# Optimization experiments

Measured on AMD Instinct MI355X. Metric: run time of the kernel, lower is better.

## Reference

```python
import jax, jax.numpy as jnp
import numpy as np

N_USER = 50000
N_ITEM = 50000
N_EDGE = 800000
D = 128


def _segment_mean(x, idx, num_segments):
    # scatter-mean: sum then divide by in-degree (0 rows stay 0, like PyG mean aggr)
    s = jax.ops.segment_sum(x, idx, num_segments=num_segments)
    cnt = jax.ops.segment_sum(jnp.ones((idx.shape[0], 1), x.dtype), idx, num_segments=num_segments)
    return s / jnp.maximum(cnt, 1.0)


def setup_inputs() -> dict:
    key = jax.random.key(0)
    ks = jax.random.split(key, 11)
    inp = {
        "user_ids": jax.random.randint(ks[0], (N_USER,), 0, N_USER),
        "item_x": jax.random.normal(ks[1], (N_ITEM, D), dtype=jnp.float32),
        "edge_ui": jax.random.randint(ks[2], (2, N_EDGE), 0, N_USER),  # row0: user src, row1: item dst
        "edge_iu": jax.random.randint(ks[3], (2, N_EDGE), 0, N_ITEM),  # row0: item src, row1: user dst
        "user_emb": jax.random.normal(ks[4], (N_USER, D), dtype=jnp.float32),
        "W_l_ui": jax.random.normal(ks[5], (D, D), dtype=jnp.float32) * 0.05,
        "W_r_ui": jax.random.normal(ks[6], (D, D), dtype=jnp.float32) * 0.05,
        "b_ui": jnp.zeros((D,), dtype=jnp.float32),
        "W_l_iu": jax.random.normal(ks[7], (D, D), dtype=jnp.float32) * 0.05,
        "W_r_iu": jax.random.normal(ks[8], (D, D), dtype=jnp.float32) * 0.05,
        "b_iu": jnp.zeros((D,), dtype=jnp.float32),
    }
    return inp


def reference(user_ids, item_x, edge_ui, edge_iu, user_emb,
              W_l_ui, W_r_ui, b_ui, W_l_iu, W_r_iu, b_iu):
    # Embedding lookup for transductive node type 'user'
    x_user = user_emb[user_ids]  # [N_USER, D]

    # SAGEConv for edge type (user -> rates -> item):
    # out_item = lin_l(mean_{j in N(i)} x_user[j]) + lin_r(item_x[i]) + bias
    msg_ui = x_user[edge_ui[0]]                    # gather src features [E, D]
    agg_ui = _segment_mean(msg_ui, edge_ui[1], N_ITEM)
    out_item = agg_ui @ W_l_ui + item_x @ W_r_ui + b_ui

    # SAGEConv for edge type (item -> rev_rates -> user)
    msg_iu = item_x[edge_iu[0]]
    agg_iu = _segment_mean(msg_iu, edge_iu[1], N_USER)
    out_user = agg_iu @ W_l_iu + x_user @ W_r_iu + b_iu

    # HeteroConv aggr='mean' across edge types: each node type is the target of
    # exactly one edge type here, so the cross-edge-type mean is the identity.
    return (out_user, out_item)
```

## Files before the change

### kernel.cpp

```cpp
#include <hip/hip_runtime.h>

#define N_USER 50000
#define N_ITEM 50000
#define N_EDGE 800000
#define D 128
#define NTOT   100000
#define NE2    1600000
#define BKT_SH 9
#define NBKT   196
#define CAP    12288
#define SLOT   10240

typedef __attribute__((ext_vector_type(8))) short     bf16x8;
typedef __attribute__((ext_vector_type(4))) float     f32x4;
typedef __attribute__((ext_vector_type(4))) unsigned short ushortx4;
typedef __attribute__((ext_vector_type(8))) unsigned short ushortx8;

__device__ __forceinline__ unsigned short f2bf(float f) {
    unsigned int u = __float_as_uint(f);
    unsigned int r = (u + 0x7fffu + ((u >> 16) & 1u)) >> 16;
    return (unsigned short)r;
}
__device__ __forceinline__ float bf2f(unsigned short b) {
    return __uint_as_float(((unsigned int)b) << 16);
}

#define SCAT_BLOCKS  196
#define PACK_BLOCKS  3125
#define PACKW_BLOCKS 8

__global__ __launch_bounds__(1024) void scatterpack_kernel(
    const float* __restrict__ user_emb, const int* __restrict__ user_ids,
    const float* __restrict__ item_x,
    const int* __restrict__ edge_ui, const int* __restrict__ edge_iu,
    const float* __restrict__ Wl_ui, const float* __restrict__ Wr_ui,
    const float* __restrict__ Wl_iu, const float* __restrict__ Wr_iu,
    unsigned short* T_user, unsigned short* T_item,
    unsigned short* WfragUI, unsigned short* WfragIU,
    int* __restrict__ bcur, unsigned int* __restrict__ records)
{
    const int b = blockIdx.x;
    const int tid = threadIdx.x;

    if (b < SCAT_BLOCKS) {
        __shared__ int bcnt[NBKT];
        __shared__ int bpos[NBKT];
        for (int i = tid; i < NBKT; i += 1024) bcnt[i] = 0;
        __syncthreads();

        const int e0 = b * 8192;
        unsigned int rec[8];
        int bkt[8], rnk[8];
#pragma unroll
        for (int j = 0; j < 8; ++j) {
            int e = e0 + j * 1024 + tid;
            bkt[j] = -1;
            if (e < NE2) {
                int s, d;
                if (e < N_EDGE) { s = edge_ui[e]; d = edge_ui[N_EDGE + e]; }
                else { int f = e - N_EDGE; s = edge_iu[f]; d = N_ITEM + edge_iu[N_EDGE + f]; }
                bkt[j] = d >> BKT_SH;
                rec[j] = (unsigned int)s | ((unsigned int)(d & 511) << 16);
                rnk[j] = atomicAdd(&bcnt[bkt[j]], 1);
            }
        }
        __syncthreads();
        for (int i = tid; i < NBKT; i += 1024) {
            int c = bcnt[i];
            bpos[i] = i * SLOT + (c ? atomicAdd(&bcur[i], c) : 0);
        }
        __syncthreads();
#pragma unroll
        for (int j = 0; j < 8; ++j) {
            if (bkt[j] >= 0) {
                int p = bpos[bkt[j]] + rnk[j];
                if (p < (bkt[j] + 1) * SLOT) records[p] = rec[j];
            }
        }
    } else if (b < SCAT_BLOCKS + PACK_BLOCKS) {
        int gid = (b - SCAT_BLOCKS) * 1024 + tid;
        int row = gid >> 5;
        int c = (gid & 31) << 2;
        const float* src;
        unsigned short* dst;
        if (row < N_USER) {
            src = user_emb + (size_t)user_ids[row] * D;
            dst = T_user + (size_t)row * 128;
        } else {
            int r = row - N_USER;
            src = item_x + (size_t)r * D;
            dst = T_item + (size_t)r * 128;
        }
        const float4 v = *reinterpret_cast<const float4*>(src + c);
        ushortx4 o;
        o.x = f2bf(v.x); o.y = f2bf(v.y); o.z = f2bf(v.z); o.w = f2bf(v.w);
        *reinterpret_cast<ushortx4*>(dst + c) = o;
    } else {
        int id = (b - SCAT_BLOCKS - PACK_BLOCKS) * 1024 + tid;
        const float *Wl, *Wr;
        unsigned short* Wf;
        if (id < 4096) { Wl = Wl_ui; Wr = Wr_ui; Wf = WfragUI; }
        else { id -= 4096; Wl = Wl_iu; Wr = Wr_iu; Wf = WfragIU; }
        int lane = id & 63;
        int c    = (id >> 6) & 7;
        int ks   = id >> 9;
        int col  = c * 16 + (lane & 15);
        int k0   = ks * 32 + (lane >> 4) * 8;
        ushortx8 o;
#pragma unroll
        for (int i = 0; i < 8; ++i) {
            int k = k0 + i;
            float f = (k < D) ? Wl[(size_t)k * D + col] : Wr[(size_t)(k - D) * D + col];
            o[i] = f2bf(f);
        }
        *reinterpret_cast<ushortx8*>(Wf + (size_t)id * 8) = o;
    }
}

__global__ __launch_bounds__(1024) void csr_build_kernel(
    const unsigned int* __restrict__ records, const int* __restrict__ bcur,
    unsigned short* __restrict__ csr, uint2* __restrict__ offdeg)
{
    __shared__ int dcnt[512];
    __shared__ int sa[512], sb[512];
    __shared__ int dcur[512];
    __shared__ unsigned short stage[CAP];

    const int b    = blockIdx.x;
    const int tid  = threadIdx.x;
    const int base = b * SLOT;
    int nb = bcur[b];
    if (nb > SLOT) nb = SLOT;

    if (tid < 512) dcnt[tid] = 0;
    __syncthreads();

    for (int i = tid; i < nb; i += 1024)
        atomicAdd(&dcnt[records[base + i] >> 16], 1);
    __syncthreads();

    int* pa = sa; int* pb = sb;
    if (tid < 512) pa[tid] = dcnt[tid];
    __syncthreads();
    for (int d = 1; d < 512; d <<= 1) {
        if (tid < 512) pb[tid] = pa[tid] + ((tid >= d) ? pa[tid - d] : 0);
        __syncthreads();
        int* t = pa; pa = pb; pb = t;
    }
    if (tid < 512) {
        int excl = pa[tid] - dcnt[tid];
        dcur[tid] = excl;
        int dst = b * 512 + tid;
        if (dst < NTOT) offdeg[dst] = make_uint2((unsigned int)(base + excl),
                                                 (unsigned int)dcnt[tid]);
    }
    __syncthreads();

    if (nb <= CAP) {
        for (int i = tid; i < nb; i += 1024) {
            unsigned int r = records[base + i];
            int p = atomicAdd(&dcur[r >> 16], 1);
            stage[p] = (unsigned short)r;
        }
        __syncthreads();
        for (int i = tid; i < nb; i += 1024) csr[base + i] = stage[i];
    } else {
        for (int i = tid; i < nb; i += 1024) {
            unsigned int r = records[base + i];
            int p = atomicAdd(&dcur[r >> 16], 1);
            csr[base + p] = (unsigned short)r;
        }
    }
}

__global__ __launch_bounds__(256) void agg2c_kernel(
    const unsigned short* __restrict__ T_user, const unsigned short* __restrict__ T_item,
    const uint2* __restrict__ offdeg, const unsigned short* __restrict__ csr,
    unsigned short* __restrict__ dout_u16)
{
    int r = (blockIdx.x * blockDim.x + threadIdx.x) >> 6;
    if (r >= NTOT) return;
    const int lane = threadIdx.x & 63;
    const unsigned short* Tg;
    unsigned short* outp;
    if (r < N_ITEM) { Tg = T_user; outp = dout_u16 + (size_t)(N_USER + r) * 256; }
    else            { Tg = T_item; outp = dout_u16 + (size_t)(r - N_ITEM) * 256; }

    const uint2 od = offdeg[r];
    const int o0 = (int)od.x;
    const int deg = (int)od.y;
    const int o1 = o0 + deg;
    const int co = lane * 2;
    float ax = 0.f, ay = 0.f;
    int i = o0;

    for (; i + 15 < o1; i += 16) {
        int cv = csr[i + (lane & 15)];
        unsigned int w[16];
#pragma unroll
        for (int p = 0; p < 16; ++p) {
            int s = __builtin_amdgcn_readlane(cv, p);
            w[p] = *reinterpret_cast<const unsigned int*>(Tg + (size_t)s * 128 + co);
        }
#pragma unroll
        for (int p = 0; p < 16; ++p) {
            ax += bf2f((unsigned short)w[p]);
            ay += bf2f((unsigned short)(w[p] >> 16));
        }
    }

    int rem = o1 - i;
    if (rem > 0) {
        int cv = csr[i + (lane & 15)];
        int bl = 0;
        if (rem >= 8) {
            unsigned int w[8];
#pragma unroll
            for (int p = 0; p < 8; ++p) {
                int s = __builtin_amdgcn_readlane(cv, p);
                w[p] = *reinterpret_cast<const unsigned int*>(Tg + (size_t)s * 128 + co);
            }
#pragma unroll
            for (int p = 0; p < 8; ++p) {
                ax += bf2f((unsigned short)w[p]);
                ay += bf2f((unsigned short)(w[p] >> 16));
            }
            bl = 8; rem -= 8;
        }
        if (rem >= 4) {
            unsigned int w[4];
#pragma unroll
            for (int p = 0; p < 4; ++p) {
                int s = __builtin_amdgcn_readlane(cv, bl + p);
                w[p] = *reinterpret_cast<const unsigned int*>(Tg + (size_t)s * 128 + co);
            }
#pragma unroll
            for (int p = 0; p < 4; ++p) {
                ax += bf2f((unsigned short)w[p]);
                ay += bf2f((unsigned short)(w[p] >> 16));
            }
            bl += 4; rem -= 4;
        }
        if (rem >= 2) {
            int s0 = __builtin_amdgcn_readlane(cv, bl);
            int s1 = __builtin_amdgcn_readlane(cv, bl + 1);
            unsigned int w0 = *reinterpret_cast<const unsigned int*>(Tg + (size_t)s0 * 128 + co);
            unsigned int w1 = *reinterpret_cast<const unsigned int*>(Tg + (size_t)s1 * 128 + co);
            ax += bf2f((unsigned short)w0) + bf2f((unsigned short)w1);
            ay += bf2f((unsigned short)(w0 >> 16)) + bf2f((unsigned short)(w1 >> 16));
            bl += 2; rem -= 2;
        }
        if (rem >= 1) {
            int s = __builtin_amdgcn_readlane(cv, bl);
            unsigned int w = *reinterpret_cast<const unsigned int*>(Tg + (size_t)s * 128 + co);
            ax += bf2f((unsigned short)w);
            ay += bf2f((unsigned short)(w >> 16));
        }
    }

    float sc = (deg > 0) ? 1.0f / (float)deg : 0.0f;
    unsigned int outw = (unsigned int)f2bf(ax * sc) | ((unsigned int)f2bf(ay * sc) << 16);
    *reinterpret_cast<unsigned int*>(outp + co) = outw;
}

#define NB_FIN 782

__global__ __launch_bounds__(256) void finish2c_kernel(
    unsigned short* dout_u16,
    const unsigned short* __restrict__ T_user, const unsigned short* __restrict__ T_item,
    const unsigned short* __restrict__ WfragUI, const unsigned short* __restrict__ WfragIU,
    const float* __restrict__ b_ui, const float* __restrict__ b_iu)
{
    const int b = blockIdx.x;
    const unsigned short *headBase, *Ts, *Wfrag;
    const float* bias;
    float* outp;
    int rowBase;
    if (b < NB_FIN) {
        headBase = dout_u16 + (size_t)N_USER * 256;
        Ts = T_item; Wfrag = WfragUI; bias = b_ui;
        outp = reinterpret_cast<float*>(dout_u16) + (size_t)N_USER * 128;
        rowBase = b * 64;
    } else {
        headBase = dout_u16;
        Ts = T_user; Wfrag = WfragIU; bias = b_iu;
        outp = reinterpret_cast<float*>(dout_u16);
        rowBase = (b - NB_FIN) * 64;
    }

    const int tid  = threadIdx.x;
    const int wave = tid >> 6;
    const int lane = tid & 63;
    const int kg   = lane >> 4;
    rowBase += wave * 16;

    int arow = rowBase + (lane & 15);
    int arow_c = (arow < 50000) ? arow : 49999;
    const unsigned short* head_ptr = headBase + (size_t)arow_c * 256 + kg * 8;
    const unsigned short* tail_ptr = Ts + (size_t)arow_c * 128 + kg * 8;

    f32x4 acc[8];
#pragma unroll
    for (int c = 0; c < 8; ++c) acc[c] = (f32x4){0.f, 0.f, 0.f, 0.f};

#pragma unroll
    for (int ks = 0; ks < 8; ++ks) {
        bf16x8 a;
        if (ks < 4) a = *reinterpret_cast<const bf16x8*>(head_ptr + ks * 32);
        else        a = *reinterpret_cast<const bf16x8*>(tail_ptr + (ks - 4) * 32);
        const unsigned short* bptr = Wfrag + ((size_t)(ks * 8) * 64 + lane) * 8;
#pragma unroll
        for (int c = 0; c < 8; ++c) {
            bf16x8 bb = *reinterpret_cast<const bf16x8*>(bptr + (size_t)c * 512);
            acc[c] = __builtin_amdgcn_mfma_f32_16x16x32_bf16(a, bb, acc[c], 0, 0, 0);
        }
    }

    const int orow0 = rowBase + kg * 4;
    const int ocol  = lane & 15;
#pragma unroll
    for (int c = 0; c < 8; ++c) {
        float bv = bias[c * 16 + ocol];
#pragma unroll
        for (int r = 0; r < 4; ++r) {
            int row = orow0 + r;
            if (row < 50000) outp[(size_t)row * 128 + c * 16 + ocol] = acc[c][r] + bv;
        }
    }
}

extern "C" void kernel_launch(void* const* d_in, const int* in_sizes, int n_in,
                              void* d_out, int out_size, void* d_ws, size_t ws_size,
                              hipStream_t stream) {
    const int*   user_ids = (const int*)d_in[0];
    const float* item_x   = (const float*)d_in[1];
    const int*   edge_ui  = (const int*)d_in[2];
    const int*   edge_iu  = (const int*)d_in[3];
    const float* user_emb = (const float*)d_in[4];
    const float* W_l_ui   = (const float*)d_in[5];
    const float* W_r_ui   = (const float*)d_in[6];
    const float* b_ui     = (const float*)d_in[7];
    const float* W_l_iu   = (const float*)d_in[8];
    const float* W_r_iu   = (const float*)d_in[9];
    const float* b_iu     = (const float*)d_in[10];

    unsigned short* dout_u16 = (unsigned short*)d_out;

    unsigned short* WfragUI = (unsigned short*)d_ws;
    unsigned short* WfragIU = WfragUI + 32768;
    unsigned short* T_user  = WfragIU + 32768;
    unsigned short* T_item  = T_user + (size_t)N_USER * 128;
    unsigned int*   records = (unsigned int*)(T_item + (size_t)N_ITEM * 128);
    unsigned short* csr     = (unsigned short*)(records + (size_t)NBKT * SLOT);
    uint2* offdeg = (uint2*)(csr + (size_t)NBKT * SLOT + 16);
    int*   bcur   = (int*)(offdeg + NTOT);

    hipMemsetAsync(bcur, 0, NBKT * sizeof(int), stream);

    scatterpack_kernel<<<SCAT_BLOCKS + PACK_BLOCKS + PACKW_BLOCKS, 1024, 0, stream>>>(
        user_emb, user_ids, item_x, edge_ui, edge_iu,
        W_l_ui, W_r_ui, W_l_iu, W_r_iu,
        T_user, T_item, WfragUI, WfragIU, bcur, records);
    csr_build_kernel<<<NBKT, 1024, 0, stream>>>(records, bcur, csr, offdeg);
    agg2c_kernel<<<(NTOT * 64) / 256, 256, 0, stream>>>(T_user, T_item, offdeg, csr, dout_u16);
    finish2c_kernel<<<2 * NB_FIN, 256, 0, stream>>>(
        dout_u16, T_user, T_item, WfragUI, WfragIU, b_ui, b_iu);
}
```

Before: 121.6 us.

## Split bf16 feature tables into 32-column quarter planes for cache-local gathers

The packed bf16 node tables are stored as four column-quarter planes (each 64 B per row) instead of 256 B rows. The aggregation kernel now gives each block one column quarter and one row group, with four edges gathered per wave instruction (16 lanes per edge) and a cross-lane reduction at the end. The aim is to shrink each gathered table slice so it stays resident in cache across blocks working on the same quarter. The cost is a larger grid of 100000 blocks, extra shuffles and a reduction step, and the finish kernel has to read the tail operand from the strided plane layout.

```diff
diff --git a/kernel.cpp b/kernel.cpp
--- a/kernel.cpp
+++ b/kernel.cpp
@@ -10,6 +10,7 @@
 #define NBKT   196
 #define CAP    12288
 #define SLOT   10240
+#define QSTRIDE (50000 * 32)
 
 typedef __attribute__((ext_vector_type(8))) short     bf16x8;
 typedef __attribute__((ext_vector_type(4))) float     f32x4;
@@ -80,21 +81,17 @@
     } else if (b < SCAT_BLOCKS + PACK_BLOCKS) {
         int gid = (b - SCAT_BLOCKS) * 1024 + tid;
         int row = gid >> 5;
-        int c = (gid & 31) << 2;
+        int c0 = (gid & 31) << 2;
         const float* src;
-        unsigned short* dst;
-        if (row < N_USER) {
-            src = user_emb + (size_t)user_ids[row] * D;
-            dst = T_user + (size_t)row * 128;
-        } else {
-            int r = row - N_USER;
-            src = item_x + (size_t)r * D;
-            dst = T_item + (size_t)r * 128;
-        }
-        const float4 v = *reinterpret_cast<const float4*>(src + c);
+        unsigned short* T;
+        int trow;
+        if (row < N_USER) { src = user_emb + (size_t)user_ids[row] * D; T = T_user; trow = row; }
+        else              { src = item_x + (size_t)(row - N_USER) * D;  T = T_item; trow = row - N_USER; }
+        const float4 v = *reinterpret_cast<const float4*>(src + c0);
         ushortx4 o;
         o.x = f2bf(v.x); o.y = f2bf(v.y); o.z = f2bf(v.z); o.w = f2bf(v.w);
-        *reinterpret_cast<ushortx4*>(dst + c) = o;
+        unsigned short* dst = T + (size_t)(c0 >> 5) * QSTRIDE + (size_t)trow * 32 + (c0 & 31);
+        *reinterpret_cast<ushortx4*>(dst) = o;
     } else {
         int id = (b - SCAT_BLOCKS - PACK_BLOCKS) * 1024 + tid;
         const float *Wl, *Wr;
@@ -173,94 +170,94 @@
     }
 }
 
-__global__ __launch_bounds__(256) void agg2c_kernel(
+__global__ __launch_bounds__(256) void agg5_kernel(
     const unsigned short* __restrict__ T_user, const unsigned short* __restrict__ T_item,
     const uint2* __restrict__ offdeg, const unsigned short* __restrict__ csr,
     unsigned short* __restrict__ dout_u16)
 {
-    int r = (blockIdx.x * blockDim.x + threadIdx.x) >> 6;
-    if (r >= NTOT) return;
+    const int b    = blockIdx.x;
+    const int cls  = b & 7;
+    const int side = cls >> 2;
+    const int q    = cls & 3;
+    const int rg   = b >> 3;
+    const int wave = threadIdx.x >> 6;
     const int lane = threadIdx.x & 63;
-    const unsigned short* Tg;
-    unsigned short* outp;
-    if (r < N_ITEM) { Tg = T_user; outp = dout_u16 + (size_t)(N_USER + r) * 256; }
-    else            { Tg = T_item; outp = dout_u16 + (size_t)(r - N_ITEM) * 256; }
-
-    const uint2 od = offdeg[r];
+    const int eo   = lane >> 4;
+    const int dl   = lane & 15;
+
+    const int r = rg * 4 + wave;
+    const unsigned short* Tg = (side ? T_item : T_user) + (size_t)q * QSTRIDE;
+    const int dr = side ? (N_ITEM + r) : r;
+    unsigned short* outp = side ? (dout_u16 + (size_t)r * 256)
+                                : (dout_u16 + (size_t)(N_USER + r) * 256);
+
+    const uint2 od = offdeg[dr];
     const int o0 = (int)od.x;
     const int deg = (int)od.y;
     const int o1 = o0 + deg;
-    const int co = lane * 2;
+    const int doff = dl * 2;
     float ax = 0.f, ay = 0.f;
     int i = o0;
 
-    for (; i + 15 < o1; i += 16) {
-        int cv = csr[i + (lane & 15)];
-        unsigned int w[16];
-#pragma unroll
-        for (int p = 0; p < 16; ++p) {
-            int s = __builtin_amdgcn_readlane(cv, p);
-            w[p] = *reinterpret_cast<const unsigned int*>(Tg + (size_t)s * 128 + co);
-        }
-#pragma unroll
-        for (int p = 0; p < 16; ++p) {
-            ax += bf2f((unsigned short)w[p]);
-            ay += bf2f((unsigned short)(w[p] >> 16));
-        }
-    }
-
+    for (; i + 31 < o1; i += 32) {
+        int cv0 = csr[i + dl];
+        int cv1 = csr[i + 16 + dl];
+        unsigned int w[8];
+#pragma unroll
+        for (int g = 0; g < 4; ++g) {
+            int s = __shfl(cv0, g * 4 + eo);
+            w[g] = *reinterpret_cast<const unsigned int*>(Tg + (size_t)s * 32 + doff);
+        }
+#pragma unroll
+        for (int g = 0; g < 4; ++g) {
+            int s = __shfl(cv1, g * 4 + eo);
+            w[4 + g] = *reinterpret_cast<const unsigned int*>(Tg + (size_t)s * 32 + doff);
+        }
+#pragma unroll
+        for (int g = 0; g < 8; ++g) {
+            ax += bf2f((unsigned short)w[g]);
+            ay += bf2f((unsigned short)(w[g] >> 16));
+        }
+    }
+    if (i + 15 < o1) {
+        int cv = csr[i + dl];
+        unsigned int w[4];
+#pragma unroll
+        for (int g = 0; g < 4; ++g) {
+            int s = __shfl(cv, g * 4 + eo);
+            w[g] = *reinterpret_cast<const unsigned int*>(Tg + (size_t)s * 32 + doff);
+        }
+#pragma unroll
+        for (int g = 0; g < 4; ++g) {
+            ax += bf2f((unsigned short)w[g]);
+            ay += bf2f((unsigned short)(w[g] >> 16));
+        }
+        i += 16;
+    }
     int rem = o1 - i;
     if (rem > 0) {
-        int cv = csr[i + (lane & 15)];
-        int bl = 0;
-        if (rem >= 8) {
-            unsigned int w[8];
-#pragma unroll
-            for (int p = 0; p < 8; ++p) {
-                int s = __builtin_amdgcn_readlane(cv, p);
-                w[p] = *reinterpret_cast<const unsigned int*>(Tg + (size_t)s * 128 + co);
+        int cv = csr[i + dl];
+#pragma unroll
+        for (int g = 0; g < 4; ++g) {
+            if (g * 4 < rem) {
+                int s = __shfl(cv, g * 4 + eo);
+                unsigned int w = *reinterpret_cast<const unsigned int*>(Tg + (size_t)s * 32 + doff);
+                if (g * 4 + eo < rem) {
+                    ax += bf2f((unsigned short)w);
+                    ay += bf2f((unsigned short)(w >> 16));
+                }
             }
-#pragma unroll
-            for (int p = 0; p < 8; ++p) {
-                ax += bf2f((unsigned short)w[p]);
-                ay += bf2f((unsigned short)(w[p] >> 16));
-            }
-            bl = 8; rem -= 8;
-        }
-        if (rem >= 4) {
-            unsigned int w[4];
-#pragma unroll
-            for (int p = 0; p < 4; ++p) {
-                int s = __builtin_amdgcn_readlane(cv, bl + p);
-                w[p] = *reinterpret_cast<const unsigned int*>(Tg + (size_t)s * 128 + co);
-            }
-#pragma unroll
-            for (int p = 0; p < 4; ++p) {
-                ax += bf2f((unsigned short)w[p]);
-                ay += bf2f((unsigned short)(w[p] >> 16));
-            }
-            bl += 4; rem -= 4;
-        }
-        if (rem >= 2) {
-            int s0 = __builtin_amdgcn_readlane(cv, bl);
-            int s1 = __builtin_amdgcn_readlane(cv, bl + 1);
-            unsigned int w0 = *reinterpret_cast<const unsigned int*>(Tg + (size_t)s0 * 128 + co);
-            unsigned int w1 = *reinterpret_cast<const unsigned int*>(Tg + (size_t)s1 * 128 + co);
-            ax += bf2f((unsigned short)w0) + bf2f((unsigned short)w1);
-            ay += bf2f((unsigned short)(w0 >> 16)) + bf2f((unsigned short)(w1 >> 16));
-            bl += 2; rem -= 2;
-        }
-        if (rem >= 1) {
-            int s = __builtin_amdgcn_readlane(cv, bl);
-            unsigned int w = *reinterpret_cast<const unsigned int*>(Tg + (size_t)s * 128 + co);
-            ax += bf2f((unsigned short)w);
-            ay += bf2f((unsigned short)(w >> 16));
-        }
-    }
+        }
+    }
+
+    ax += __shfl_xor(ax, 16); ay += __shfl_xor(ay, 16);
+    ax += __shfl_xor(ax, 32); ay += __shfl_xor(ay, 32);
 
     float sc = (deg > 0) ? 1.0f / (float)deg : 0.0f;
-    unsigned int outw = (unsigned int)f2bf(ax * sc) | ((unsigned int)f2bf(ay * sc) << 16);
-    *reinterpret_cast<unsigned int*>(outp + co) = outw;
+    if (eo == 0) {
+        unsigned int outw = (unsigned int)f2bf(ax * sc) | ((unsigned int)f2bf(ay * sc) << 16);
+        *reinterpret_cast<unsigned int*>(outp + q * 32 + doff) = outw;
+    }
 }
 
 #define NB_FIN 782
@@ -297,7 +294,6 @@
     int arow = rowBase + (lane & 15);
     int arow_c = (arow < 50000) ? arow : 49999;
     const unsigned short* head_ptr = headBase + (size_t)arow_c * 256 + kg * 8;
-    const unsigned short* tail_ptr = Ts + (size_t)arow_c * 128 + kg * 8;
 
     f32x4 acc[8];
 #pragma unroll
@@ -306,8 +302,12 @@
 #pragma unroll
     for (int ks = 0; ks < 8; ++ks) {
         bf16x8 a;
-        if (ks < 4) a = *reinterpret_cast<const bf16x8*>(head_ptr + ks * 32);
-        else        a = *reinterpret_cast<const bf16x8*>(tail_ptr + (ks - 4) * 32);
+        if (ks < 4) {
+            a = *reinterpret_cast<const bf16x8*>(head_ptr + ks * 32);
+        } else {
+            a = *reinterpret_cast<const bf16x8*>(
+                Ts + (size_t)(ks - 4) * QSTRIDE + (size_t)arow_c * 32 + kg * 8);
+        }
         const unsigned short* bptr = Wfrag + ((size_t)(ks * 8) * 64 + lane) * 8;
 #pragma unroll
         for (int c = 0; c < 8; ++c) {
@@ -349,8 +349,8 @@
     unsigned short* WfragUI = (unsigned short*)d_ws;
     unsigned short* WfragIU = WfragUI + 32768;
     unsigned short* T_user  = WfragIU + 32768;
-    unsigned short* T_item  = T_user + (size_t)N_USER * 128;
-    unsigned int*   records = (unsigned int*)(T_item + (size_t)N_ITEM * 128);
+    unsigned short* T_item  = T_user + (size_t)4 * QSTRIDE;
+    unsigned int*   records = (unsigned int*)(T_item + (size_t)4 * QSTRIDE);
     unsigned short* csr     = (unsigned short*)(records + (size_t)NBKT * SLOT);
     uint2* offdeg = (uint2*)(csr + (size_t)NBKT * SLOT + 16);
     int*   bcur   = (int*)(offdeg + NTOT);
@@ -362,7 +362,7 @@
         W_l_ui, W_r_ui, W_l_iu, W_r_iu,
         T_user, T_item, WfragUI, WfragIU, bcur, records);
     csr_build_kernel<<<NBKT, 1024, 0, stream>>>(records, bcur, csr, offdeg);
-    agg2c_kernel<<<(NTOT * 64) / 256, 256, 0, stream>>>(T_user, T_item, offdeg, csr, dout_u16);
+    agg5_kernel<<<100000, 256, 0, stream>>>(T_user, T_item, offdeg, csr, dout_u16);
     finish2c_kernel<<<2 * NB_FIN, 256, 0, stream>>>(
         dout_u16, T_user, T_item, WfragUI, WfragIU, b_ui, b_iu);
 }
```

Result: slower. 177.9 us (+46.3%).
